# Kernel optimization log

Measured on AMD Instinct MI355X. Metric: run time of the kernel, lower is better.

## Reference

```python
import jax, jax.numpy as jnp
import numpy as np

B, D, H, S, E = 16384, 512, 1024, 8, 4
DH = D // 2  # attention hidden


def setup_inputs() -> dict:
    key = jax.random.key(0)
    ks = jax.random.split(key, 20)
    std = 0.1
    return {
        "x": jax.random.normal(ks[0], (B, D), jnp.float32),
        "scenario_ids": jax.random.randint(ks[1], (B,), 0, S, jnp.int32),
        # shared SEI gate
        "gate_w": jax.random.normal(ks[2], (D, E), jnp.float32) * std,
        "gate_b": jnp.zeros((E,), jnp.float32),
        # shared sub-experts (stacked): D -> H -> D
        "sub_w1": jax.random.normal(ks[3], (E, D, H), jnp.float32) * std,
        "sub_b1": jnp.zeros((E, H), jnp.float32),
        "sub_w2": jax.random.normal(ks[4], (E, H, D), jnp.float32) * std,
        "sub_b2": jnp.zeros((E, D), jnp.float32),
        # scenario-specific experts (stacked): D -> H -> D
        "spec_w1": jax.random.normal(ks[5], (S, D, H), jnp.float32) * std,
        "spec_b1": jnp.zeros((S, H), jnp.float32),
        "spec_w2": jax.random.normal(ks[6], (S, H, D), jnp.float32) * std,
        "spec_b2": jnp.zeros((S, D), jnp.float32),
        # SAN scenario embeddings + attention MLP (2D -> D/2 -> 1)
        "scen_embed": jax.random.normal(ks[7], (S, D), jnp.float32) * std,
        "attn_w1": jax.random.normal(ks[8], (2 * D, DH), jnp.float32) * std,
        "attn_b1": jnp.zeros((DH,), jnp.float32),
        "attn_w2": jax.random.normal(ks[9], (DH, 1), jnp.float32) * std,
        "attn_b2": jnp.zeros((1,), jnp.float32),
        # SAN output projection (4D -> D)
        "out_w": jax.random.normal(ks[10], (4 * D, D), jnp.float32) * std,
        "out_b": jnp.zeros((D,), jnp.float32),
    }


def reference(x, scenario_ids, gate_w, gate_b, sub_w1, sub_b1, sub_w2, sub_b2,
              spec_w1, spec_b1, spec_w2, spec_b2, scen_embed,
              attn_w1, attn_b1, attn_w2, attn_b2, out_w, out_b):
    b = x.shape[0]
    # --- shared expert (SEI): softmax-gated mixture of E sub-experts ---
    gates = jax.nn.softmax(x @ gate_w + gate_b, axis=-1)            # [B,E]
    h = jax.nn.relu(jnp.einsum('bd,edh->ebh', x, sub_w1) + sub_b1[:, None, :])
    exp_out = jnp.einsum('ebh,ehd->ebd', h, sub_w2) + sub_b2[:, None, :]
    shared = jnp.einsum('be,ebd->bd', gates, exp_out)               # [B,D]
    # --- scenario-specific experts: run all, gather per-sample ---
    hs = jax.nn.relu(jnp.einsum('bd,sdh->sbh', x, spec_w1) + spec_b1[:, None, :])
    spec_all = jnp.einsum('sbh,shd->sbd', hs, spec_w2) + spec_b2[:, None, :]  # [S,B,D]
    specific = spec_all[scenario_ids, jnp.arange(b)]                # [B,D]
    # --- scenario-aware attention (SAN) ---
    # logits[s,b] = MLP(cat([shared[b], scen_embed[s]]))
    s = scen_embed.shape[0]
    comb = jnp.concatenate([
        jnp.broadcast_to(shared[None], (s, b, shared.shape[-1])),
        jnp.broadcast_to(scen_embed[:, None, :], (s, b, scen_embed.shape[-1])),
    ], axis=-1)                                                      # [S,B,2D]
    ah = jax.nn.relu(comb @ attn_w1 + attn_b1)                       # [S,B,D/2]
    logits = (ah @ attn_w2 + attn_b2)[..., 0]                        # [S,B]
    attn_w = jax.nn.softmax(logits.T, axis=-1)                       # [B,S]
    # in the original, all non-current scenario reprs are zeros, so the
    # weighted sums reduce to w[b, sid[b]] * (shared/specific)
    wsel = jnp.take_along_axis(attn_w, scenario_ids[:, None], axis=1)  # [B,1]
    enhanced = jnp.concatenate([shared, wsel * shared, specific, wsel * specific], axis=-1)
    return enhanced @ out_w + out_b                                  # [B,D]
```

## Files before the change

kernel.cpp:

```cpp
#include <hip/hip_runtime.h>
#include <hip/hip_bf16.h>
#include <stdint.h>

typedef __hip_bfloat16 bf16;
typedef __attribute__((ext_vector_type(8))) short short8;
typedef __attribute__((ext_vector_type(4))) short short4v;
typedef __attribute__((ext_vector_type(4))) float f32x4;

constexpr int cB = 16384, cD = 512, cH = 1024, cS = 8, cE = 4, cDH = 256;

__device__ __forceinline__ float tof(bf16 v) { return __bfloat162float(v); }
__device__ __forceinline__ bf16 tob(float v) { return __float2bfloat16(v); }
__device__ __forceinline__ float b2f(short s) {
  uint32_t u = ((uint32_t)(uint16_t)s) << 16;
  return __builtin_bit_cast(float, u);
}
__device__ __forceinline__ float ldf(const void* p, long i, int isbf) {
  return isbf ? b2f(((const short*)p)[i]) : ((const float*)p)[i];
}

__device__ __forceinline__ void gload_lds16(const bf16* g, char* l) {
  __builtin_amdgcn_global_load_lds(
      (const __attribute__((address_space(1))) void*)g,
      (__attribute__((address_space(3))) void*)l, 16, 0, 0);
}

__global__ __launch_bounds__(256) void probe_k(const void* x, int* flag) {
  __shared__ int sh[256];
  const unsigned short* u = (const unsigned short*)x;
  int cnt = 0;
  for (int i = threadIdx.x; i < 2048; i += 256) {
    float v = fabsf(b2f((short)u[2 * i]));
    cnt += (v > 1e-5f && v < 1e3f) ? 1 : 0;
  }
  sh[threadIdx.x] = cnt;
  __syncthreads();
  for (int s = 128; s > 0; s >>= 1) {
    if (threadIdx.x < s) sh[threadIdx.x] += sh[threadIdx.x + s];
    __syncthreads();
  }
  if (threadIdx.x == 0) flag[0] = (sh[0] > 1024) ? 1 : 0;
}

__global__ __launch_bounds__(256) void cvtx_k(const void* x, bf16* xb, const int* flag) {
  int g = blockIdx.x * 256 + threadIdx.x;
  if (flag[0]) {
    ((short8*)xb)[g] = ((const short8*)x)[g];
  } else {
    const f32x4* xf = (const f32x4*)x;
    f32x4 v0 = xf[2 * g], v1 = xf[2 * g + 1];
    short8 o;
#pragma unroll
    for (int j = 0; j < 4; j++) {
      o[j] = __builtin_bit_cast(short, tob(v0[j]));
      o[j + 4] = __builtin_bit_cast(short, tob(v1[j]));
    }
    ((short8*)xb)[g] = o;
  }
}

struct CvtDesc {
  const void* src[11];
  int off[12];
};
__global__ __launch_bounds__(256) void cvt_smalls_k(CvtDesc d, const int* flag, float* dst) {
  int i = blockIdx.x * 256 + threadIdx.x;
  if (i >= d.off[11]) return;
  int isb = flag[0];
  int j = 0;
  while (i >= d.off[j + 1]) j++;
  dst[i] = ldf(d.src[j], i - d.off[j], isb);
}

__global__ __launch_bounds__(256) void transpose_k(const void* in, bf16* out, int ldin, int ldout,
                                                   long in_off, long in_bs, long out_bs,
                                                   const int* flag) {
  __shared__ float tile[32][33];
  int isb = flag[0];
  long src0 = in_off + (long)blockIdx.z * in_bs;
  bf16* dst = out + (long)blockIdx.z * out_bs;
  int c0 = blockIdx.x * 32, r0 = blockIdx.y * 32;
  int tx = threadIdx.x & 31, ty = threadIdx.x >> 5;
#pragma unroll
  for (int i = 0; i < 4; i++)
    tile[ty + i * 8][tx] = ldf(in, src0 + (long)(r0 + ty + i * 8) * ldin + c0 + tx, isb);
  __syncthreads();
#pragma unroll
  for (int i = 0; i < 4; i++)
    dst[(long)(c0 + ty + i * 8) * ldout + r0 + tx] = tob(tile[tx][ty + i * 8]);
}

struct GArgs {
  const bf16* A; int lda;
  const bf16* Bt; int ldb; long bt_stride;
  void* C; int ldc;
  int M, N, K;
  const float* bias; int bias_stride;
  const float* gates; int eidx;
  const int* perm; const int* cum;
  const bf16* P1; const float* wsel;
  const int* dflag;
};

template <int EPI, bool GROUPED, bool GATHER_A, bool SCATTER_C>
__global__ __launch_bounds__(256, 4) void gemm_k(GArgs a) {
  __shared__ char smem[32768];
  char* ldsA = smem;
  char* ldsB = smem + 16384;

  int bxs, bys;
  if constexpr (!GROUPED) {
    const int gx = gridDim.x;
    const int nwg = gx * gridDim.y;
    const int d = blockIdx.y * gx + blockIdx.x;
    const int q = nwg >> 3, r = nwg & 7;
    const int xcd = d & 7, di = d >> 3;
    const int logical = (xcd < r ? xcd * (q + 1) : r * (q + 1) + (xcd - r) * q) + di;
    bxs = logical % gx;
    bys = logical / gx;
  } else {
    bxs = blockIdx.x;
    bys = blockIdx.y;
  }

  int g0, cnt;
  if constexpr (GROUPED) {
    int z = blockIdx.z;
    g0 = a.cum[z];
    cnt = a.cum[z + 1] - g0;
  } else {
    g0 = 0;
    cnt = a.M;
  }
  const int ptile = bys * 128;
  if (ptile >= cnt) return;
  const int n0 = bxs * 128;

  const int t = threadIdx.x, w = t >> 6, l = t & 63;
  const int wm = w >> 1, wn = w & 1;

  const bf16* bt = a.Bt + (GROUPED ? (long)blockIdx.z * a.bt_stride : 0);
  const float* bias = a.bias ? (a.bias + (GROUPED ? blockIdx.z * a.bias_stride : 0)) : nullptr;

  const bf16* aSrc[4];
  const bf16* bSrc[4];
  int ldsOff[4];
#pragma unroll
  for (int c = 0; c < 4; c++) {
    int pos = w * 4096 + c * 1024 + l * 16;
    int row = pos >> 7;
    int su = ((((pos >> 4) & 7) ^ (row & 7))) * 8;
    int p = ptile + row;
    if (p > cnt - 1) p = cnt - 1;
    int ar;
    if constexpr (GATHER_A) ar = a.perm[g0 + p];
    else ar = g0 + p;
    aSrc[c] = a.A + (long)ar * a.lda + su;
    bSrc[c] = bt + (long)(n0 + row) * a.ldb + su;
    ldsOff[c] = w * 4096 + c * 1024;
  }

  f32x4 zero = {0.f, 0.f, 0.f, 0.f};
  f32x4 acc[4][4];
#pragma unroll
  for (int i = 0; i < 4; i++)
#pragma unroll
    for (int j = 0; j < 4; j++) acc[i][j] = zero;

  const int nkt = a.K >> 6;
  for (int kt = 0; kt < nkt; ++kt) {
#pragma unroll
    for (int c = 0; c < 4; c++) gload_lds16(aSrc[c] + kt * 64, ldsA + ldsOff[c]);
#pragma unroll
    for (int c = 0; c < 4; c++) gload_lds16(bSrc[c] + kt * 64, ldsB + ldsOff[c]);
    __syncthreads();
#pragma unroll
    for (int kk = 0; kk < 2; kk++) {
      short8 af[4], bv[4];
#pragma unroll
      for (int mi = 0; mi < 4; mi++) {
        int row = wm * 64 + mi * 16 + (l & 15);
        int kg = kk * 4 + (l >> 4);
        int off = row * 128 + ((kg ^ (row & 7)) << 4);
        af[mi] = *(const short8*)(ldsA + off);
      }
#pragma unroll
      for (int ni = 0; ni < 4; ni++) {
        int row = wn * 64 + ni * 16 + (l & 15);
        int kg = kk * 4 + (l >> 4);
        int off = row * 128 + ((kg ^ (row & 7)) << 4);
        bv[ni] = *(const short8*)(ldsB + off);
      }
#pragma unroll
      for (int mi = 0; mi < 4; mi++)
#pragma unroll
        for (int ni = 0; ni < 4; ni++)
          acc[mi][ni] =
              __builtin_amdgcn_mfma_f32_16x16x32_bf16(af[mi], bv[ni], acc[mi][ni], 0, 0, 0);
    }
    __syncthreads();
  }

  const int l15 = l & 15, lg4 = l >> 4;
  int outbf = 1;
  if constexpr (EPI == 5) outbf = a.dflag[0];
#pragma unroll
  for (int mi = 0; mi < 4; mi++) {
#pragma unroll
    for (int j = 0; j < 4; j++) {
      int p = ptile + wm * 64 + mi * 16 + lg4 * 4 + j;
      if (p >= cnt) continue;
      int crow;
      if constexpr (SCATTER_C) crow = a.perm[g0 + p];
      else crow = g0 + p;
#pragma unroll
      for (int ni = 0; ni < 4; ni++) {
        int n = n0 + wn * 64 + ni * 16 + l15;
        float v = acc[mi][ni][j];
        if constexpr (EPI == 1) {
          v += bias[n];
          v = fmaxf(v, 0.f);
          ((bf16*)a.C)[(long)crow * a.ldc + n] = tob(v);
        } else if constexpr (EPI == 2) {
          float g = a.gates[(long)(g0 + p) * 4 + a.eidx];
          v = g * (v + bias[n]);
          float* Cf = (float*)a.C;
          long idx = (long)crow * a.ldc + n;
          if (a.eidx == 0) Cf[idx] = v;
          else Cf[idx] += v;
        } else if constexpr (EPI == 3) {
          ((float*)a.C)[(long)crow * a.ldc + n] = v;
        } else if constexpr (EPI == 4) {
          v += bias[n];
          ((bf16*)a.C)[(long)crow * a.ldc + n] = tob(v);
        } else if constexpr (EPI == 5) {
          float o = tof(a.P1[(long)crow * a.N + n]) + a.wsel[crow] * v + bias[n];
          if (outbf) ((bf16*)a.C)[(long)crow * a.ldc + n] = tob(o);
          else ((float*)a.C)[(long)crow * a.ldc + n] = o;
        } else if constexpr (EPI == 6) {
          float g = a.gates[(long)(g0 + p) * 4 + (n >> 10)];
          v = g * fmaxf(v + bias[n], 0.f);
          ((bf16*)a.C)[(long)crow * a.ldc + n] = tob(v);
        } else if constexpr (EPI == 7) {
          const float* gr = a.gates + (long)(g0 + p) * 4;
          v += gr[0] * bias[n] + gr[1] * bias[512 + n] + gr[2] * bias[1024 + n] +
               gr[3] * bias[1536 + n];
          ((bf16*)a.C)[(long)crow * a.ldc + n] = tob(v);
        } else if constexpr (EPI == 8) {
          ((bf16*)a.C)[(long)crow * a.ldc + n] = tob(v);
        }
      }
    }
  }
}


__global__ __launch_bounds__(256) void gates_k(const bf16* x, const float* gw, const float* gb,
                                               float* gates) {
  int b = blockIdx.x * 4 + (threadIdx.x >> 6);
  int l = threadIdx.x & 63;
  short8 xv = *(const short8*)(x + (long)b * cD + l * 8);
  float a0 = 0, a1 = 0, a2 = 0, a3 = 0;
#pragma unroll
  for (int j = 0; j < 8; j++) {
    float xf = b2f(xv[j]);
    f32x4 wr = *(const f32x4*)(gw + (l * 8 + j) * 4);
    a0 += xf * wr[0];
    a1 += xf * wr[1];
    a2 += xf * wr[2];
    a3 += xf * wr[3];
  }
#pragma unroll
  for (int o = 32; o > 0; o >>= 1) {
    a0 += __shfl_xor(a0, o);
    a1 += __shfl_xor(a1, o);
    a2 += __shfl_xor(a2, o);
    a3 += __shfl_xor(a3, o);
  }
  a0 += gb[0];
  a1 += gb[1];
  a2 += gb[2];
  a3 += gb[3];
  float m = fmaxf(fmaxf(a0, a1), fmaxf(a2, a3));
  float e0 = expf(a0 - m), e1 = expf(a1 - m), e2 = expf(a2 - m), e3 = expf(a3 - m);
  float s = e0 + e1 + e2 + e3;
  if (l == 0) {
    float* gp = gates + (long)b * 4;
    gp[0] = e0 / s;
    gp[1] = e1 / s;
    gp[2] = e2 / s;
    gp[3] = e3 / s;
  }
}

__global__ __launch_bounds__(256) void bhist_k(const int* sid, int* bh) {
  int blk = blockIdx.x, t = threadIdx.x;
  __shared__ int h[cS];
  if (t < cS) h[t] = 0;
  __syncthreads();
  int s = sid[blk * 256 + t];
#pragma unroll
  for (int q = 0; q < cS; q++) {
    unsigned long long m = __ballot(s == q);
    if ((t & 63) == 0) atomicAdd(&h[q], __popcll(m));
  }
  __syncthreads();
  if (t < cS) bh[blk * cS + t] = h[t];
}

__global__ void bbase_k(const int* bh, int* base, int* cum) {
  __shared__ int tot[cS];
  int s = threadIdx.x;
  if (s < cS) {
    int run = 0;
    for (int b = 0; b < 64; b++) {
      base[b * cS + s] = run;
      run += bh[b * cS + s];
    }
    tot[s] = run;
  }
  __syncthreads();
  if (s == 0) {
    int run = 0;
    for (int q = 0; q < cS; q++) {
      cum[q] = run;
      run += tot[q];
    }
    cum[cS] = run;
  }
  __syncthreads();
  if (s < cS) {
    int c = cum[s];
    for (int b = 0; b < 64; b++) base[b * cS + s] += c;
  }
}

__global__ __launch_bounds__(256) void bscat_k(const int* sid, const int* base, int* perm) {
  int blk = blockIdx.x, t = threadIdx.x, w = t >> 6, l = t & 63;
// ... 33 lines not shown
  red[dg][nl] = a;
  __syncthreads();
  if (dg == 0) {
    float t = b1[n];
#pragma unroll
    for (int g = 0; g < 8; g++) t += red[g][nl];
    scp[s * cDH + n] = t;
  }
}

__global__ __launch_bounds__(256) void wsel_k(const float* sp, const float* scp, const float* w2,
                                              const int* sid, float* wsel) {
  int b = blockIdx.x * 4 + (threadIdx.x >> 6);
  int l = threadIdx.x & 63;
  float spv[4], w2v[4];
#pragma unroll
  for (int q = 0; q < 4; q++) {
    spv[q] = sp[(long)b * cDH + q * 64 + l];
    w2v[q] = w2[q * 64 + l];
  }
  float lg[8];
#pragma unroll
  for (int s = 0; s < 8; s++) {
    float acc = 0.f;
#pragma unroll
    for (int q = 0; q < 4; q++) {
      float v = spv[q] + scp[s * cDH + q * 64 + l];
      v = fmaxf(v, 0.f);
      acc += v * w2v[q];
    }
#pragma unroll
    for (int o = 32; o > 0; o >>= 1) acc += __shfl_xor(acc, o);
    lg[s] = acc;
  }
  float m = lg[0];
#pragma unroll
  for (int s = 1; s < 8; s++) m = fmaxf(m, lg[s]);
  float sum = 0.f;
#pragma unroll
  for (int s = 0; s < 8; s++) sum += expf(lg[s] - m);
  if (l == 0) {
    int s0 = sid[b];
    wsel[b] = expf(lg[s0] - m) / sum;
  }
}

__global__ __launch_bounds__(256) void cvt_shared_k(const float* sf, bf16* ss) {
  int i = blockIdx.x * 256 + threadIdx.x;
  int r = i >> 7, c = (i & 127) * 4;
  f32x4 v = *(const f32x4*)(sf + (long)r * cD + c);
  short4v o;
#pragma unroll
  for (int j = 0; j < 4; j++) o[j] = __builtin_bit_cast(short, tob(v[j]));
  *(short4v*)(ss + (long)r * 1024 + c) = o;
}

extern "C" void kernel_launch(void* const* d_in, const int* in_sizes, int n_in, void* d_out,
                              int out_size, void* d_ws, size_t ws_size, hipStream_t stream) {
  const void* x = d_in[0];
  const int* sid = (const int*)d_in[1];

  char* ws = (char*)d_ws;
  size_t off = 0;
  auto alloc = [&](size_t bytes) -> void* {
    void* p = ws + off;
    off += (bytes + 255) & ~(size_t)255;
    return p;
  };
  int* g_flag = (int*)alloc(64);
  float* g_gates = (float*)alloc((size_t)cB * 4 * 4);
  float* g_wsel = (float*)alloc((size_t)cB * 4);
  int* g_perm = (int*)alloc((size_t)cB * 4);
  int* g_bh = (int*)alloc(64 * cS * 4);
  int* g_base = (int*)alloc(64 * cS * 4);
  int* g_cum = (int*)alloc(64);
  float* g_scp = (float*)alloc((size_t)cS * cDH * 4);
  float* g_small = (float*)alloc((size_t)300000 * 4);
  bf16* g_xb = (bf16*)alloc((size_t)cB * cD * 2);
  bf16* w1t = (bf16*)alloc((size_t)cE * cH * cD * 2);
  bf16* w2cat = (bf16*)alloc((size_t)cD * 4096 * 2);
  bf16* s1t = (bf16*)alloc((size_t)cS * cH * cD * 2);
  bf16* s2t = (bf16*)alloc((size_t)cS * cD * cH * 2);
  bf16* a1t = (bf16*)alloc((size_t)cDH * cD * 2);
  bf16* ow1t = (bf16*)alloc((size_t)cD * 1024 * 2);
  bf16* ow2t = (bf16*)alloc((size_t)cD * 1024 * 2);
  bf16* g_ss = (bf16*)alloc((size_t)cB * 1024 * 2);
  size_t fixed_end = off;
  const size_t MB = 1024ull * 1024ull;
  const bool BIG = (ws_size == 0) || (fixed_end + 135 * MB <= ws_size);
  char* g_big = (char*)alloc(BIG ? 135 * MB : 85 * MB);
  (void)in_sizes;
  (void)n_in;
  (void)out_size;

  dim3 blk(256);
  probe_k<<<1, blk, 0, stream>>>(x, g_flag);
  cvtx_k<<<cB * cD / 8 / 256, blk, 0, stream>>>(x, g_xb, g_flag);

  const int O_GW = 0, O_GB = 2048, O_SB1 = 2052, O_SB2 = 6148, O_PB1 = 8196, O_PB2 = 16388,
            O_EMB = 20484, O_AW1 = 24580, O_AB1 = 286724, O_AW2 = 286980, O_OB = 287236,
            O_END = 287748;
  {
    CvtDesc d;
    const void* srcs[11] = {d_in[2],  d_in[3],  d_in[5],  d_in[7],  d_in[9], d_in[11],
                            d_in[12], d_in[13], d_in[14], d_in[15], d_in[18]};
    int offs[12] = {O_GW, O_GB, O_SB1, O_SB2, O_PB1, O_PB2, O_EMB, O_AW1, O_AB1, O_AW2, O_OB,
                    O_END};
    for (int i = 0; i < 11; i++) d.src[i] = srcs[i];
    for (int i = 0; i < 12; i++) d.off[i] = offs[i];
    cvt_smalls_k<<<(O_END + 255) / 256, blk, 0, stream>>>(d, g_flag, g_small);
  }

  transpose_k<<<dim3(cH / 32, cD / 32, cE), blk, 0, stream>>>(d_in[4], w1t, cH, cD, 0,
                                                              (long)cD * cH, (long)cH * cD, g_flag);
  transpose_k<<<dim3(cD / 32, cH / 32, cE), blk, 0, stream>>>(d_in[6], w2cat, cD, 4096, 0,
                                                              (long)cH * cD, 1024, g_flag);
  transpose_k<<<dim3(cH / 32, cD / 32, cS), blk, 0, stream>>>(d_in[8], s1t, cH, cD, 0,
                                                              (long)cD * cH, (long)cH * cD, g_flag);
  transpose_k<<<dim3(cD / 32, cH / 32, cS), blk, 0, stream>>>(d_in[10], s2t, cD, cH, 0,
                                                              (long)cH * cD, (long)cD * cH, g_flag);
  transpose_k<<<dim3(cDH / 32, cD / 32, 1), blk, 0, stream>>>(d_in[13], a1t, cDH, cD, 0, 0, 0,
                                                              g_flag);
  transpose_k<<<dim3(cD / 32, cD / 32, 1), blk, 0, stream>>>(d_in[17], ow1t, cD, 1024, 0, 0, 0,
                                                             g_flag);
  transpose_k<<<dim3(cD / 32, cD / 32, 1), blk, 0, stream>>>(d_in[17], ow1t + 512, cD, 1024,
                                                             (long)1024 * cD, 0, 0, g_flag);
  transpose_k<<<dim3(cD / 32, cD / 32, 1), blk, 0, stream>>>(d_in[17], ow2t, cD, 1024,
                                                             (long)512 * cD, 0, 0, g_flag);
  transpose_k<<<dim3(cD / 32, cD / 32, 1), blk, 0, stream>>>(d_in[17], ow2t + 512, cD, 1024,
                                                             (long)1536 * cD, 0, 0, g_flag);

  gates_k<<<cB / 4, blk, 0, stream>>>(g_xb, g_small + O_GW, g_small + O_GB, g_gates);
  bhist_k<<<cB / 256, blk, 0, stream>>>(sid, g_bh);
  bbase_k<<<1, 64, 0, stream>>>(g_bh, g_base, g_cum);
  bscat_k<<<cB / 256, blk, 0, stream>>>(sid, g_base, g_perm);

  if (BIG) {
    bf16* h4 = (bf16*)g_big;
    float* sp = (float*)g_big;
    bf16* hspec = (bf16*)g_big;
    bf16* P1 = (bf16*)(g_big + 34 * MB);
    {
      GArgs a{};
      a.A = g_xb; a.lda = cD;
      a.Bt = w1t; a.ldb = cD;
      a.C = h4; a.ldc = 4096;
      a.M = cB; a.N = 4096; a.K = cD;
      a.bias = g_small + O_SB1;
      a.gates = g_gates;
      gemm_k<6, false, false, false><<<dim3(32, cB / 128), blk, 0, stream>>>(a);
    }
    {
      GArgs a{};
      a.A = h4; a.lda = 4096;
      a.Bt = w2cat; a.ldb = 4096;
      a.C = g_ss; a.ldc = 1024;
      a.M = cB; a.N = cD; a.K = 4096;
      a.bias = g_small + O_SB2;
      a.gates = g_gates;
      gemm_k<7, false, false, false><<<dim3(cD / 128, cB / 128), blk, 0, stream>>>(a);
    }
    {
      GArgs a{};
      a.A = g_ss; a.lda = 1024;
      a.Bt = a1t; a.ldb = cD;
      a.C = sp; a.ldc = cDH;
      a.M = cB; a.N = cDH; a.K = cD;
      gemm_k<3, false, false, false><<<dim3(cDH / 128, cB / 128), blk, 0, stream>>>(a);
    }
    scenpart_k<<<dim3(cS, 8), blk, 0, stream>>>(g_small + O_EMB, g_small + O_AW1, g_small + O_AB1,
                                                g_scp);
    wsel_k<<<cB / 4, blk, 0, stream>>>(sp, g_scp, g_small + O_AW2, sid, g_wsel);
    {
      GArgs a{};
      a.A = g_xb; a.lda = cD;
      a.Bt = s1t; a.ldb = cD; a.bt_stride = (long)cH * cD;
      a.C = hspec; a.ldc = cH;
      a.M = cB; a.N = cH; a.K = cD;
      a.bias = g_small + O_PB1; a.bias_stride = cH;
      a.perm = g_perm; a.cum = g_cum;
      gemm_k<1, true, true, false><<<dim3(cH / 128, cB / 128, cS), blk, 0, stream>>>(a);
    }
    {
      GArgs a{};
      a.A = hspec; a.lda = cH;
      a.Bt = s2t; a.ldb = cH; a.bt_stride = (long)cD * cH;
      a.C = g_ss + 512; a.ldc = 1024;
      a.M = cB; a.N = cD; a.K = cH;
      a.bias = g_small + O_PB2; a.bias_stride = cD;
      a.perm = g_perm; a.cum = g_cum;
      gemm_k<4, true, false, true><<<dim3(cD / 128, cB / 128, cS), blk, 0, stream>>>(a);
    }
    {
      GArgs a{};
      a.A = g_ss; a.lda = 1024;
      a.Bt = ow1t; a.ldb = 1024;
      a.C = P1; a.ldc = cD;
      a.M = cB; a.N = cD; a.K = 1024;
      gemm_k<8, false, false, false><<<dim3(cD / 128, cB / 128), blk, 0, stream>>>(a);
    }
    {
      GArgs a{};
      a.A = g_ss; a.lda = 1024;
      a.Bt = ow2t; a.ldb = 1024;
      a.C = d_out; a.ldc = cD;
      a.M = cB; a.N = cD; a.K = 1024;
      a.bias = g_small + O_OB;
      a.P1 = P1; a.wsel = g_wsel; a.dflag = g_flag;
      gemm_k<5, false, false, false><<<dim3(cD / 128, cB / 128), blk, 0, stream>>>(a);
    }
  } else {
    float* f32a = (float*)g_big;
    bf16* hbuf = (bf16*)(g_big + 34 * MB);
    bf16* P1b = (bf16*)(g_big + 68 * MB);
    for (int e = 0; e < cE; e++) {
      GArgs a1{};
      a1.A = g_xb; a1.lda = cD;
      a1.Bt = w1t + (size_t)e * cH * cD; a1.ldb = cD;
      a1.C = hbuf; a1.ldc = cH;
      a1.M = cB; a1.N = cH; a1.K = cD;
      a1.bias = g_small + O_SB1 + e * cH;
      gemm_k<1, false, false, false><<<dim3(cH / 128, cB / 128), blk, 0, stream>>>(a1);
      GArgs a2{};
      a2.A = hbuf; a2.lda = cH;
      a2.Bt = w2cat + (size_t)e * 1024; a2.ldb = 4096;
      a2.C = f32a; a2.ldc = cD;
      a2.M = cB; a2.N = cD; a2.K = cH;
      a2.bias = g_small + O_SB2 + e * cD;
      a2.gates = g_gates; a2.eidx = e;
      gemm_k<2, false, false, false><<<dim3(cD / 128, cB / 128), blk, 0, stream>>>(a2);
    }
    cvt_shared_k<<<cB * 128 / 256, blk, 0, stream>>>(f32a, g_ss);
    {
      GArgs a{};
      a.A = g_xb; a.lda = cD;
      a.Bt = s1t; a.ldb = cD; a.bt_stride = (long)cH * cD;
      a.C = hbuf; a.ldc = cH;
      a.M = cB; a.N = cH; a.K = cD;
      a.bias = g_small + O_PB1; a.bias_stride = cH;
      a.perm = g_perm; a.cum = g_cum;
      gemm_k<1, true, true, false><<<dim3(cH / 128, cB / 128, cS), blk, 0, stream>>>(a);
    }
    {
      GArgs a{};
      a.A = hbuf; a.lda = cH;
      a.Bt = s2t; a.ldb = cH; a.bt_stride = (long)cD * cH;
      a.C = g_ss + 512; a.ldc = 1024;
      a.M = cB; a.N = cD; a.K = cH;
      a.bias = g_small + O_PB2; a.bias_stride = cD;
      a.perm = g_perm; a.cum = g_cum;
      gemm_k<4, true, false, true><<<dim3(cD / 128, cB / 128, cS), blk, 0, stream>>>(a);
    }
    {
      GArgs a{};
      a.A = g_ss; a.lda = 1024;
      a.Bt = a1t; a.ldb = cD;
      a.C = f32a; a.ldc = cDH;
      a.M = cB; a.N = cDH; a.K = cD;
      gemm_k<3, false, false, false><<<dim3(cDH / 128, cB / 128), blk, 0, stream>>>(a);
    }
    scenpart_k<<<dim3(cS, 8), blk, 0, stream>>>(g_small + O_EMB, g_small + O_AW1, g_small + O_AB1,
                                                g_scp);
    wsel_k<<<cB / 4, blk, 0, stream>>>(f32a, g_scp, g_small + O_AW2, sid, g_wsel);
    {
      GArgs a{};
      a.A = g_ss; a.lda = 1024;
      a.Bt = ow1t; a.ldb = 1024;
      a.C = P1b; a.ldc = cD;
      a.M = cB; a.N = cD; a.K = 1024;
      gemm_k<8, false, false, false><<<dim3(cD / 128, cB / 128), blk, 0, stream>>>(a);
    }
    {
      GArgs a{};
      a.A = g_ss; a.lda = 1024;
      a.Bt = ow2t; a.ldb = 1024;
      a.C = d_out; a.ldc = cD;
      a.M = cB; a.N = cD; a.K = 1024;
      a.bias = g_small + O_OB;
      a.P1 = P1b; a.wsel = g_wsel; a.dflag = g_flag;
      gemm_k<5, false, false, false><<<dim3(cD / 128, cB / 128), blk, 0, stream>>>(a);
    }
  }
}
```

Baseline: 460.9 us.

## Add 256x256-tile 512-thread GEMM kernel for dense stages with XCD remap

Adds a new GEMM kernel using 256x256 output tiles, 8 waves, double-buffered direct-to-LDS loads with XOR swizzle, priority-boosted MFMA blocks and an XCD-aware workgroup remapping. It replaces the 128x128 GEMMs for the shared-expert up/down projections and the two output-projection GEMMs on the big-workspace path. Larger tiles raise arithmetic intensity and cut redundant global traffic. The cost is 128KB LDS, one block per CU, and fewer blocks (128 for N=512 GEMMs), which may underfill the GPU.

```diff
diff --git a/kernel.cpp b/kernel.cpp
--- a/kernel.cpp
+++ b/kernel.cpp
@@ -254,6 +254,177 @@
   }
 }
 
+struct G6Args {
+  const bf16* A;
+  const bf16* Bt;
+  void* C;
+  int N, K, ldc;
+  const float* bias;
+  const float* gates;
+  const bf16* P1;
+  const float* wsel;
+  const int* dflag;
+};
+
+template <int EPI>
+__global__ __launch_bounds__(512, 1) void gemm256_k(G6Args a) {
+  extern __shared__ char sm[];
+  const int t = threadIdx.x, w = t >> 6, l = t & 63;
+  const int wm = w >> 2, wn = w & 3;
+
+  const int gx = gridDim.x;
+  const int nwg = gx * gridDim.y;
+  const int d = blockIdx.y * gx + blockIdx.x;
+  const int q = nwg >> 3, r = nwg & 7;
+  const int xcd = d & 7, di = d >> 3;
+  const int logical = (xcd < r ? xcd * (q + 1) : r * (q + 1) + (xcd - r) * q) + di;
+  const int m0 = (logical / gx) * 256, n0 = (logical % gx) * 256;
+
+  const bf16* aS[4];
+  const bf16* bS[4];
+  int ldsO[4];
+#pragma unroll
+  for (int c = 0; c < 4; c++) {
+    int pos = c * 8192 + t * 16;
+    int row = pos >> 7;
+    int su = (((pos >> 4) & 7) ^ (row & 7)) * 8;
+    aS[c] = a.A + (long)(m0 + row) * a.K + su;
+    bS[c] = a.Bt + (long)(n0 + row) * a.K + su;
+    ldsO[c] = c * 8192 + (w << 10);
+  }
+  auto stage = [&](int kt, int bb) {
+#pragma unroll
+    for (int c = 0; c < 4; c++) gload_lds16(aS[c] + kt * 64, sm + bb * 65536 + ldsO[c]);
+#pragma unroll
+    for (int c = 0; c < 4; c++) gload_lds16(bS[c] + kt * 64, sm + bb * 65536 + 32768 + ldsO[c]);
+  };
+  auto rdA = [&](int bb, int mi, int kk) -> short8 {
+    int row = wm * 128 + mi * 16 + (l & 15);
+    int kg = kk * 4 + (l >> 4);
+    return *(const short8*)(sm + bb * 65536 + row * 128 + ((kg ^ (row & 7)) << 4));
+  };
+  auto rdB = [&](int bb, int ni, int kk) -> short8 {
+    int row = wn * 64 + ni * 16 + (l & 15);
+    int kg = kk * 4 + (l >> 4);
+    return *(const short8*)(sm + bb * 65536 + 32768 + row * 128 + ((kg ^ (row & 7)) << 4));
+  };
+
+  f32x4 acc[8][4];
+#pragma unroll
+  for (int i = 0; i < 8; i++)
+#pragma unroll
+    for (int j = 0; j < 4; j++) acc[i][j] = {0.f, 0.f, 0.f, 0.f};
+
+  const int nkt = a.K >> 6;
+  stage(0, 0);
+  stage(1, 1);
+
+  for (int kt = 0; kt < nkt; ++kt) {
+    const int bb = kt & 1;
+    if (kt + 1 < nkt) {
+      asm volatile("s_waitcnt vmcnt(8)" ::: "memory");
+    } else {
+      asm volatile("s_waitcnt vmcnt(0)" ::: "memory");
+    }
+    __builtin_amdgcn_sched_barrier(0);
+    __builtin_amdgcn_s_barrier();
+    __builtin_amdgcn_sched_barrier(0);
+
+    short8 fa[4][2], fb0[2][2], fb1[2][2];
+#pragma unroll
+    for (int mi = 0; mi < 4; mi++)
+#pragma unroll
+      for (int kk = 0; kk < 2; kk++) fa[mi][kk] = rdA(bb, mi, kk);
+#pragma unroll
+    for (int ni = 0; ni < 2; ni++)
+#pragma unroll
+      for (int kk = 0; kk < 2; kk++) fb0[ni][kk] = rdB(bb, ni, kk);
+    __builtin_amdgcn_s_setprio(1);
+#pragma unroll
+    for (int mi = 0; mi < 4; mi++)
+#pragma unroll
+      for (int ni = 0; ni < 2; ni++)
+#pragma unroll
+        for (int kk = 0; kk < 2; kk++)
+          acc[mi][ni] = __builtin_amdgcn_mfma_f32_16x16x32_bf16(fa[mi][kk], fb0[ni][kk],
+                                                                acc[mi][ni], 0, 0, 0);
+    __builtin_amdgcn_s_setprio(0);
+#pragma unroll
+    for (int ni = 0; ni < 2; ni++)
+#pragma unroll
+      for (int kk = 0; kk < 2; kk++) fb1[ni][kk] = rdB(bb, ni + 2, kk);
+    __builtin_amdgcn_s_setprio(1);
+#pragma unroll
+    for (int mi = 0; mi < 4; mi++)
+#pragma unroll
+      for (int ni = 0; ni < 2; ni++)
+#pragma unroll
+        for (int kk = 0; kk < 2; kk++)
+          acc[mi][ni + 2] = __builtin_amdgcn_mfma_f32_16x16x32_bf16(fa[mi][kk], fb1[ni][kk],
+                                                                    acc[mi][ni + 2], 0, 0, 0);
+    __builtin_amdgcn_s_setprio(0);
+#pragma unroll
+    for (int mi = 0; mi < 4; mi++)
+#pragma unroll
+      for (int kk = 0; kk < 2; kk++) fa[mi][kk] = rdA(bb, mi + 4, kk);
+    __builtin_amdgcn_s_setprio(1);
+#pragma unroll
+    for (int mi = 0; mi < 4; mi++)
+#pragma unroll
+      for (int ni = 0; ni < 2; ni++)
+#pragma unroll
+        for (int kk = 0; kk < 2; kk++)
+          acc[mi + 4][ni] = __builtin_amdgcn_mfma_f32_16x16x32_bf16(fa[mi][kk], fb0[ni][kk],
+                                                                    acc[mi + 4][ni], 0, 0, 0);
+    __builtin_amdgcn_s_setprio(0);
+    __builtin_amdgcn_s_setprio(1);
+#pragma unroll
+    for (int mi = 0; mi < 4; mi++)
+#pragma unroll
+      for (int ni = 0; ni < 2; ni++)
+#pragma unroll
+        for (int kk = 0; kk < 2; kk++)
+          acc[mi + 4][ni + 2] = __builtin_amdgcn_mfma_f32_16x16x32_bf16(fa[mi][kk], fb1[ni][kk],
+                                                                        acc[mi + 4][ni + 2], 0, 0, 0);
+    __builtin_amdgcn_s_setprio(0);
+
+    __builtin_amdgcn_s_barrier();
+    __builtin_amdgcn_sched_barrier(0);
+    if (kt + 2 < nkt) stage(kt + 2, bb);
+  }
+
+  const int l15 = l & 15, lg4 = l >> 4;
+  int outbf = 1;
+  if constexpr (EPI == 5) outbf = a.dflag[0];
+#pragma unroll
+  for (int mi = 0; mi < 8; mi++) {
+#pragma unroll
+    for (int j = 0; j < 4; j++) {
+      int crow = m0 + wm * 128 + mi * 16 + lg4 * 4 + j;
+#pragma unroll
+      for (int ni = 0; ni < 4; ni++) {
+        int n = n0 + wn * 64 + ni * 16 + l15;
+        float v = acc[mi][ni][j];
+        if constexpr (EPI == 6) {
+          float g = a.gates[(long)crow * 4 + (n >> 10)];
+          v = g * fmaxf(v + a.bias[n], 0.f);
+          ((bf16*)a.C)[(long)crow * a.ldc + n] = tob(v);
+        } else if constexpr (EPI == 7) {
+          const float* gr = a.gates + (long)crow * 4;
+          v += gr[0] * a.bias[n] + gr[1] * a.bias[512 + n] + gr[2] * a.bias[1024 + n] +
+               gr[3] * a.bias[1536 + n];
+          ((bf16*)a.C)[(long)crow * a.ldc + n] = tob(v);
+        } else if constexpr (EPI == 8) {
+          ((bf16*)a.C)[(long)crow * a.ldc + n] = tob(v);
+        } else if constexpr (EPI == 5) {
+          float o = tof(a.P1[(long)crow * a.N + n]) + a.wsel[crow] * v + a.bias[n];
+          if (outbf) ((bf16*)a.C)[(long)crow * a.ldc + n] = tob(o);
+          else ((float*)a.C)[(long)crow * a.ldc + n] = o;
+        }
+      }
+    }
+  }
+}
 
 __global__ __launch_bounds__(256) void gates_k(const bf16* x, const float* gw, const float* gb,
                                                float* gates) {
@@ -464,6 +635,16 @@
   (void)n_in;
   (void)out_size;
 
+  bool use256 = true;
+  use256 &= hipFuncSetAttribute(reinterpret_cast<const void*>(gemm256_k<6>),
+                                hipFuncAttributeMaxDynamicSharedMemorySize, 131072) == hipSuccess;
+  use256 &= hipFuncSetAttribute(reinterpret_cast<const void*>(gemm256_k<7>),
+                                hipFuncAttributeMaxDynamicSharedMemorySize, 131072) == hipSuccess;
+  use256 &= hipFuncSetAttribute(reinterpret_cast<const void*>(gemm256_k<8>),
+                                hipFuncAttributeMaxDynamicSharedMemorySize, 131072) == hipSuccess;
+  use256 &= hipFuncSetAttribute(reinterpret_cast<const void*>(gemm256_k<5>),
+                                hipFuncAttributeMaxDynamicSharedMemorySize, 131072) == hipSuccess;
+
   dim3 blk(256);
   probe_k<<<1, blk, 0, stream>>>(x, g_flag);
   cvtx_k<<<cB * cD / 8 / 256, blk, 0, stream>>>(x, g_xb, g_flag);
@@ -511,32 +692,37 @@
     float* sp = (float*)g_big;
     bf16* hspec = (bf16*)g_big;
     bf16* P1 = (bf16*)(g_big + 34 * MB);
+
+    if (use256) {
+      G6Args a{};
+      a.A = g_xb; a.Bt = w1t; a.C = h4;
+      a.N = 4096; a.K = cD; a.ldc = 4096;
+      a.bias = g_small + O_SB1; a.gates = g_gates;
+      gemm256_k<6><<<dim3(16, 64), 512, 131072, stream>>>(a);
+    } else {
+      GArgs a{};
+      a.A = g_xb; a.lda = cD; a.Bt = w1t; a.ldb = cD;
+      a.C = h4; a.ldc = 4096; a.M = cB; a.N = 4096; a.K = cD;
+      a.bias = g_small + O_SB1; a.gates = g_gates;
+      gemm_k<6, false, false, false><<<dim3(32, cB / 128), blk, 0, stream>>>(a);
+    }
+    if (use256) {
+      G6Args a{};
+      a.A = h4; a.Bt = w2cat; a.C = g_ss;
+      a.N = cD; a.K = 4096; a.ldc = 1024;
+      a.bias = g_small + O_SB2; a.gates = g_gates;
+      gemm256_k<7><<<dim3(2, 64), 512, 131072, stream>>>(a);
+    } else {
+      GArgs a{};
+      a.A = h4; a.lda = 4096; a.Bt = w2cat; a.ldb = 4096;
+      a.C = g_ss; a.ldc = 1024; a.M = cB; a.N = cD; a.K = 4096;
+      a.bias = g_small + O_SB2; a.gates = g_gates;
+      gemm_k<7, false, false, false><<<dim3(cD / 128, cB / 128), blk, 0, stream>>>(a);
+    }
     {
       GArgs a{};
-      a.A = g_xb; a.lda = cD;
-      a.Bt = w1t; a.ldb = cD;
-      a.C = h4; a.ldc = 4096;
-      a.M = cB; a.N = 4096; a.K = cD;
-      a.bias = g_small + O_SB1;
-      a.gates = g_gates;
-      gemm_k<6, false, false, false><<<dim3(32, cB / 128), blk, 0, stream>>>(a);
-    }
-    {
-      GArgs a{};
-      a.A = h4; a.lda = 4096;
-      a.Bt = w2cat; a.ldb = 4096;
-      a.C = g_ss; a.ldc = 1024;
-      a.M = cB; a.N = cD; a.K = 4096;
-      a.bias = g_small + O_SB2;
-      a.gates = g_gates;
-      gemm_k<7, false, false, false><<<dim3(cD / 128, cB / 128), blk, 0, stream>>>(a);
-    }
-    {
-      GArgs a{};
-      a.A = g_ss; a.lda = 1024;
-      a.Bt = a1t; a.ldb = cD;
-      a.C = sp; a.ldc = cDH;
-      a.M = cB; a.N = cDH; a.K = cD;
+      a.A = g_ss; a.lda = 1024; a.Bt = a1t; a.ldb = cD;
+      a.C = sp; a.ldc = cDH; a.M = cB; a.N = cDH; a.K = cD;
       gemm_k<3, false, false, false><<<dim3(cDH / 128, cB / 128), blk, 0, stream>>>(a);
     }
     scenpart_k<<<dim3(cS, 8), blk, 0, stream>>>(g_small + O_EMB, g_small + O_AW1, g_small + O_AB1,
@@ -544,40 +730,42 @@
     wsel_k<<<cB / 4, blk, 0, stream>>>(sp, g_scp, g_small + O_AW2, sid, g_wsel);
     {
       GArgs a{};
-      a.A = g_xb; a.lda = cD;
-      a.Bt = s1t; a.ldb = cD; a.bt_stride = (long)cH * cD;
-      a.C = hspec; a.ldc = cH;
-      a.M = cB; a.N = cH; a.K = cD;
+      a.A = g_xb; a.lda = cD; a.Bt = s1t; a.ldb = cD; a.bt_stride = (long)cH * cD;
+      a.C = hspec; a.ldc = cH; a.M = cB; a.N = cH; a.K = cD;
       a.bias = g_small + O_PB1; a.bias_stride = cH;
       a.perm = g_perm; a.cum = g_cum;
       gemm_k<1, true, true, false><<<dim3(cH / 128, cB / 128, cS), blk, 0, stream>>>(a);
     }
     {
       GArgs a{};
-      a.A = hspec; a.lda = cH;
-      a.Bt = s2t; a.ldb = cH; a.bt_stride = (long)cD * cH;
-      a.C = g_ss + 512; a.ldc = 1024;
-      a.M = cB; a.N = cD; a.K = cH;
+      a.A = hspec; a.lda = cH; a.Bt = s2t; a.ldb = cH; a.bt_stride = (long)cD * cH;
+      a.C = g_ss + 512; a.ldc = 1024; a.M = cB; a.N = cD; a.K = cH;
       a.bias = g_small + O_PB2; a.bias_stride = cD;
       a.perm = g_perm; a.cum = g_cum;
       gemm_k<4, true, false, true><<<dim3(cD / 128, cB / 128, cS), blk, 0, stream>>>(a);
     }
-    {
-      GArgs a{};
-      a.A = g_ss; a.lda = 1024;
-      a.Bt = ow1t; a.ldb = 1024;
-      a.C = P1; a.ldc = cD;
-      a.M = cB; a.N = cD; a.K = 1024;
+    if (use256) {
+      G6Args a{};
+      a.A = g_ss; a.Bt = ow1t; a.C = P1;
+      a.N = cD; a.K = 1024; a.ldc = cD;
+      gemm256_k<8><<<dim3(2, 64), 512, 131072, stream>>>(a);
+    } else {
+      GArgs a{};
+      a.A = g_ss; a.lda = 1024; a.Bt = ow1t; a.ldb = 1024;
+      a.C = P1; a.ldc = cD; a.M = cB; a.N = cD; a.K = 1024;
       gemm_k<8, false, false, false><<<dim3(cD / 128, cB / 128), blk, 0, stream>>>(a);
     }
-    {
-      GArgs a{};
-      a.A = g_ss; a.lda = 1024;
-      a.Bt = ow2t; a.ldb = 1024;
-      a.C = d_out; a.ldc = cD;
-      a.M = cB; a.N = cD; a.K = 1024;
-      a.bias = g_small + O_OB;
-      a.P1 = P1; a.wsel = g_wsel; a.dflag = g_flag;
+    if (use256) {
+      G6Args a{};
+      a.A = g_ss; a.Bt = ow2t; a.C = d_out;
+      a.N = cD; a.K = 1024; a.ldc = cD;
+      a.bias = g_small + O_OB; a.P1 = P1; a.wsel = g_wsel; a.dflag = g_flag;
+      gemm256_k<5><<<dim3(2, 64), 512, 131072, stream>>>(a);
+    } else {
+      GArgs a{};
+      a.A = g_ss; a.lda = 1024; a.Bt = ow2t; a.ldb = 1024;
+      a.C = d_out; a.ldc = cD; a.M = cB; a.N = cD; a.K = 1024;
+      a.bias = g_small + O_OB; a.P1 = P1; a.wsel = g_wsel; a.dflag = g_flag;
       gemm_k<5, false, false, false><<<dim3(cD / 128, cB / 128), blk, 0, stream>>>(a);
     }
   } else {
@@ -586,48 +774,37 @@
     bf16* P1b = (bf16*)(g_big + 68 * MB);
     for (int e = 0; e < cE; e++) {
       GArgs a1{};
-      a1.A = g_xb; a1.lda = cD;
-      a1.Bt = w1t + (size_t)e * cH * cD; a1.ldb = cD;
-      a1.C = hbuf; a1.ldc = cH;
-      a1.M = cB; a1.N = cH; a1.K = cD;
+      a1.A = g_xb; a1.lda = cD; a1.Bt = w1t + (size_t)e * cH * cD; a1.ldb = cD;
+      a1.C = hbuf; a1.ldc = cH; a1.M = cB; a1.N = cH; a1.K = cD;
       a1.bias = g_small + O_SB1 + e * cH;
       gemm_k<1, false, false, false><<<dim3(cH / 128, cB / 128), blk, 0, stream>>>(a1);
       GArgs a2{};
-      a2.A = hbuf; a2.lda = cH;
-      a2.Bt = w2cat + (size_t)e * 1024; a2.ldb = 4096;
-      a2.C = f32a; a2.ldc = cD;
-      a2.M = cB; a2.N = cD; a2.K = cH;
-      a2.bias = g_small + O_SB2 + e * cD;
-      a2.gates = g_gates; a2.eidx = e;
+      a2.A = hbuf; a2.lda = cH; a2.Bt = w2cat + (size_t)e * 1024; a2.ldb = 4096;
+      a2.C = f32a; a2.ldc = cD; a2.M = cB; a2.N = cD; a2.K = cH;
+      a2.bias = g_small + O_SB2 + e * cD; a2.gates = g_gates; a2.eidx = e;
       gemm_k<2, false, false, false><<<dim3(cD / 128, cB / 128), blk, 0, stream>>>(a2);
     }
     cvt_shared_k<<<cB * 128 / 256, blk, 0, stream>>>(f32a, g_ss);
     {
       GArgs a{};
-      a.A = g_xb; a.lda = cD;
-      a.Bt = s1t; a.ldb = cD; a.bt_stride = (long)cH * cD;
-      a.C = hbuf; a.ldc = cH;
-      a.M = cB; a.N = cH; a.K = cD;
+      a.A = g_xb; a.lda = cD; a.Bt = s1t; a.ldb = cD; a.bt_stride = (long)cH * cD;
+      a.C = hbuf; a.ldc = cH; a.M = cB; a.N = cH; a.K = cD;
       a.bias = g_small + O_PB1; a.bias_stride = cH;
       a.perm = g_perm; a.cum = g_cum;
       gemm_k<1, true, true, false><<<dim3(cH / 128, cB / 128, cS), blk, 0, stream>>>(a);
     }
     {
       GArgs a{};
-      a.A = hbuf; a.lda = cH;
-      a.Bt = s2t; a.ldb = cH; a.bt_stride = (long)cD * cH;
-      a.C = g_ss + 512; a.ldc = 1024;
-      a.M = cB; a.N = cD; a.K = cH;
+      a.A = hbuf; a.lda = cH; a.Bt = s2t; a.ldb = cH; a.bt_stride = (long)cD * cH;
+      a.C = g_ss + 512; a.ldc = 1024; a.M = cB; a.N = cD; a.K = cH;
       a.bias = g_small + O_PB2; a.bias_stride = cD;
       a.perm = g_perm; a.cum = g_cum;
       gemm_k<4, true, false, true><<<dim3(cD / 128, cB / 128, cS), blk, 0, stream>>>(a);
     }
     {
       GArgs a{};
-      a.A = g_ss; a.lda = 1024;
-      a.Bt = a1t; a.ldb = cD;
-      a.C = f32a; a.ldc = cDH;
-      a.M = cB; a.N = cDH; a.K = cD;
+      a.A = g_ss; a.lda = 1024; a.Bt = a1t; a.ldb = cD;
+      a.C = f32a; a.ldc = cDH; a.M = cB; a.N = cDH; a.K = cD;
       gemm_k<3, false, false, false><<<dim3(cDH / 128, cB / 128), blk, 0, stream>>>(a);
     }
     scenpart_k<<<dim3(cS, 8), blk, 0, stream>>>(g_small + O_EMB, g_small + O_AW1, g_small + O_AB1,
@@ -635,20 +812,15 @@
     wsel_k<<<cB / 4, blk, 0, stream>>>(f32a, g_scp, g_small + O_AW2, sid, g_wsel);
     {
       GArgs a{};
-      a.A = g_ss; a.lda = 1024;
-      a.Bt = ow1t; a.ldb = 1024;
-      a.C = P1b; a.ldc = cD;
-      a.M = cB; a.N = cD; a.K = 1024;
+      a.A = g_ss; a.lda = 1024; a.Bt = ow1t; a.ldb = 1024;
+      a.C = P1b; a.ldc = cD; a.M = cB; a.N = cD; a.K = 1024;
       gemm_k<8, false, false, false><<<dim3(cD / 128, cB / 128), blk, 0, stream>>>(a);
     }
     {
       GArgs a{};
-      a.A = g_ss; a.lda = 1024;
-      a.Bt = ow2t; a.ldb = 1024;
-      a.C = d_out; a.ldc = cD;
-      a.M = cB; a.N = cD; a.K = 1024;
-      a.bias = g_small + O_OB;
-      a.P1 = P1b; a.wsel = g_wsel; a.dflag = g_flag;
+      a.A = g_ss; a.lda = 1024; a.Bt = ow2t; a.ldb = 1024;
+      a.C = d_out; a.ldc = cD; a.M = cB; a.N = cD; a.K = 1024;
+      a.bias = g_small + O_OB; a.P1 = P1b; a.wsel = g_wsel; a.dflag = g_flag;
       gemm_k<5, false, false, false><<<dim3(cD / 128, cB / 128), blk, 0, stream>>>(a);
     }
   }
```

Result: slower. 573.6 us (+24.5%).

## Fuse the two output-projection GEMMs using an interleaved paired weight layout

Applied to the files above, without the earlier changes.

The two output-projection GEMMs (unscaled part P1 and wsel-scaled part) become one GEMM with N=1024 over a new interleaved weight layout. Each wave's accumulator tiles then hold both halves for the same output column, so the epilogue combines them as acc0 + wsel*acc1 + bias. This removes the bf16 P1 intermediate write and read-back plus one kernel launch, and the four weight transposes are merged into a single kernel. The hidden-activation epilogues also switch to nontemporal stores, which may help or hurt depending on whether those values are re-read from cache soon after.

```diff
diff --git a/kernel.cpp b/kernel.cpp
--- a/kernel.cpp
+++ b/kernel.cpp
@@ -17,6 +17,9 @@
 }
 __device__ __forceinline__ float ldf(const void* p, long i, int isbf) {
   return isbf ? b2f(((const short*)p)[i]) : ((const float*)p)[i];
+}
+__device__ __forceinline__ void stbf_nt(bf16* p, float v) {
+  __builtin_nontemporal_store(__builtin_bit_cast(short, tob(v)), (short*)p);
 }
 
 __device__ __forceinline__ void gload_lds16(const bf16* g, char* l) {
@@ -90,6 +93,26 @@
     dst[(long)(c0 + ty + i * 8) * ldout + r0 + tx] = tob(tile[tx][ty + i * 8]);
 }
 
+__global__ __launch_bounds__(256) void owt_k(const void* ow, bf16* owpair, const int* flag) {
+  __shared__ float tile[32][33];
+  int isb = flag[0];
+  int z = blockIdx.z;
+  int m = z & 1, kb = (z >> 1) * 512;
+  long base = (long)z * 512 * cD;
+  int c0 = blockIdx.x * 32, r0 = blockIdx.y * 32;
+  int tx = threadIdx.x & 31, ty = threadIdx.x >> 5;
+#pragma unroll
+  for (int i = 0; i < 4; i++)
+    tile[ty + i * 8][tx] = ldf(ow, base + (long)(r0 + ty + i * 8) * cD + c0 + tx, isb);
+  __syncthreads();
+#pragma unroll
+  for (int i = 0; i < 4; i++) {
+    int n = c0 + ty + i * 8;
+    int R = ((n >> 6) << 7) + (((n >> 5) & 1) << 6) + (m << 5) + (((n >> 4) & 1) << 4) + (n & 15);
+    owpair[(long)R * 1024 + kb + r0 + tx] = tob(tile[tx][ty + i * 8]);
+  }
+}
+
 struct GArgs {
   const bf16* A; int lda;
   const bf16* Bt; int ldb; long bt_stride;
@@ -98,7 +121,7 @@
   const float* bias; int bias_stride;
   const float* gates; int eidx;
   const int* perm; const int* cum;
-  const bf16* P1; const float* wsel;
+  const float* wsel;
   const int* dflag;
 };
 
@@ -203,7 +226,7 @@
 
   const int l15 = l & 15, lg4 = l >> 4;
   int outbf = 1;
-  if constexpr (EPI == 5) outbf = a.dflag[0];
+  if constexpr (EPI == 9) outbf = a.dflag[0];
 #pragma unroll
   for (int mi = 0; mi < 4; mi++) {
 #pragma unroll
@@ -213,6 +236,17 @@
       int crow;
       if constexpr (SCATTER_C) crow = a.perm[g0 + p];
       else crow = g0 + p;
+      if constexpr (EPI == 9) {
+        float wv = a.wsel[crow];
+#pragma unroll
+        for (int ni = 0; ni < 2; ni++) {
+          int n = (n0 >> 1) + wn * 32 + ni * 16 + l15;
+          float o = acc[mi][ni][j] + wv * acc[mi][ni + 2][j] + a.bias[n];
+          if (outbf) ((bf16*)a.C)[(long)crow * a.ldc + n] = tob(o);
+          else ((float*)a.C)[(long)crow * a.ldc + n] = o;
+        }
+        continue;
+      }
 #pragma unroll
       for (int ni = 0; ni < 4; ni++) {
         int n = n0 + wn * 64 + ni * 16 + l15;
@@ -220,7 +254,7 @@
         if constexpr (EPI == 1) {
           v += bias[n];
           v = fmaxf(v, 0.f);
-          ((bf16*)a.C)[(long)crow * a.ldc + n] = tob(v);
+          stbf_nt(&((bf16*)a.C)[(long)crow * a.ldc + n], v);
         } else if constexpr (EPI == 2) {
           float g = a.gates[(long)(g0 + p) * 4 + a.eidx];
           v = g * (v + bias[n]);
@@ -233,27 +267,20 @@
         } else if constexpr (EPI == 4) {
           v += bias[n];
           ((bf16*)a.C)[(long)crow * a.ldc + n] = tob(v);
-        } else if constexpr (EPI == 5) {
-          float o = tof(a.P1[(long)crow * a.N + n]) + a.wsel[crow] * v + bias[n];
-          if (outbf) ((bf16*)a.C)[(long)crow * a.ldc + n] = tob(o);
-          else ((float*)a.C)[(long)crow * a.ldc + n] = o;
         } else if constexpr (EPI == 6) {
           float g = a.gates[(long)(g0 + p) * 4 + (n >> 10)];
           v = g * fmaxf(v + bias[n], 0.f);
-          ((bf16*)a.C)[(long)crow * a.ldc + n] = tob(v);
+          stbf_nt(&((bf16*)a.C)[(long)crow * a.ldc + n], v);
         } else if constexpr (EPI == 7) {
           const float* gr = a.gates + (long)(g0 + p) * 4;
           v += gr[0] * bias[n] + gr[1] * bias[512 + n] + gr[2] * bias[1024 + n] +
                gr[3] * bias[1536 + n];
           ((bf16*)a.C)[(long)crow * a.ldc + n] = tob(v);
-        } else if constexpr (EPI == 8) {
-          ((bf16*)a.C)[(long)crow * a.ldc + n] = tob(v);
         }
       }
     }
   }
 }
-
 
 __global__ __launch_bounds__(256) void gates_k(const bf16* x, const float* gw, const float* gb,
                                                float* gates) {
@@ -453,13 +480,12 @@
   bf16* s1t = (bf16*)alloc((size_t)cS * cH * cD * 2);
   bf16* s2t = (bf16*)alloc((size_t)cS * cD * cH * 2);
   bf16* a1t = (bf16*)alloc((size_t)cDH * cD * 2);
-  bf16* ow1t = (bf16*)alloc((size_t)cD * 1024 * 2);
-  bf16* ow2t = (bf16*)alloc((size_t)cD * 1024 * 2);
+  bf16* owpair = (bf16*)alloc((size_t)1024 * 1024 * 2);
   bf16* g_ss = (bf16*)alloc((size_t)cB * 1024 * 2);
   size_t fixed_end = off;
   const size_t MB = 1024ull * 1024ull;
   const bool BIG = (ws_size == 0) || (fixed_end + 135 * MB <= ws_size);
-  char* g_big = (char*)alloc(BIG ? 135 * MB : 85 * MB);
+  char* g_big = (char*)alloc(BIG ? 135 * MB : 68 * MB);
   (void)in_sizes;
   (void)n_in;
   (void)out_size;
@@ -492,14 +518,7 @@
                                                               (long)cH * cD, (long)cD * cH, g_flag);
   transpose_k<<<dim3(cDH / 32, cD / 32, 1), blk, 0, stream>>>(d_in[13], a1t, cDH, cD, 0, 0, 0,
                                                               g_flag);
-  transpose_k<<<dim3(cD / 32, cD / 32, 1), blk, 0, stream>>>(d_in[17], ow1t, cD, 1024, 0, 0, 0,
-                                                             g_flag);
-  transpose_k<<<dim3(cD / 32, cD / 32, 1), blk, 0, stream>>>(d_in[17], ow1t + 512, cD, 1024,
-                                                             (long)1024 * cD, 0, 0, g_flag);
-  transpose_k<<<dim3(cD / 32, cD / 32, 1), blk, 0, stream>>>(d_in[17], ow2t, cD, 1024,
-                                                             (long)512 * cD, 0, 0, g_flag);
-  transpose_k<<<dim3(cD / 32, cD / 32, 1), blk, 0, stream>>>(d_in[17], ow2t + 512, cD, 1024,
-                                                             (long)1536 * cD, 0, 0, g_flag);
+  owt_k<<<dim3(cD / 32, cD / 32, 4), blk, 0, stream>>>(d_in[17], owpair, g_flag);
 
   gates_k<<<cB / 4, blk, 0, stream>>>(g_xb, g_small + O_GW, g_small + O_GB, g_gates);
   bhist_k<<<cB / 256, blk, 0, stream>>>(sid, g_bh);
@@ -510,33 +529,24 @@
     bf16* h4 = (bf16*)g_big;
     float* sp = (float*)g_big;
     bf16* hspec = (bf16*)g_big;
-    bf16* P1 = (bf16*)(g_big + 34 * MB);
-    {
-      GArgs a{};
-      a.A = g_xb; a.lda = cD;
-      a.Bt = w1t; a.ldb = cD;
-      a.C = h4; a.ldc = 4096;
-      a.M = cB; a.N = 4096; a.K = cD;
-      a.bias = g_small + O_SB1;
-      a.gates = g_gates;
+    {
+      GArgs a{};
+      a.A = g_xb; a.lda = cD; a.Bt = w1t; a.ldb = cD;
+      a.C = h4; a.ldc = 4096; a.M = cB; a.N = 4096; a.K = cD;
+      a.bias = g_small + O_SB1; a.gates = g_gates;
       gemm_k<6, false, false, false><<<dim3(32, cB / 128), blk, 0, stream>>>(a);
     }
     {
       GArgs a{};
-      a.A = h4; a.lda = 4096;
-      a.Bt = w2cat; a.ldb = 4096;
-      a.C = g_ss; a.ldc = 1024;
-      a.M = cB; a.N = cD; a.K = 4096;
-      a.bias = g_small + O_SB2;
-      a.gates = g_gates;
+      a.A = h4; a.lda = 4096; a.Bt = w2cat; a.ldb = 4096;
+      a.C = g_ss; a.ldc = 1024; a.M = cB; a.N = cD; a.K = 4096;
+      a.bias = g_small + O_SB2; a.gates = g_gates;
       gemm_k<7, false, false, false><<<dim3(cD / 128, cB / 128), blk, 0, stream>>>(a);
     }
     {
       GArgs a{};
-      a.A = g_ss; a.lda = 1024;
-      a.Bt = a1t; a.ldb = cD;
-      a.C = sp; a.ldc = cDH;
-      a.M = cB; a.N = cDH; a.K = cD;
+      a.A = g_ss; a.lda = 1024; a.Bt = a1t; a.ldb = cD;
+      a.C = sp; a.ldc = cDH; a.M = cB; a.N = cDH; a.K = cD;
       gemm_k<3, false, false, false><<<dim3(cDH / 128, cB / 128), blk, 0, stream>>>(a);
     }
     scenpart_k<<<dim3(cS, 8), blk, 0, stream>>>(g_small + O_EMB, g_small + O_AW1, g_small + O_AB1,
@@ -544,90 +554,63 @@
     wsel_k<<<cB / 4, blk, 0, stream>>>(sp, g_scp, g_small + O_AW2, sid, g_wsel);
     {
       GArgs a{};
-      a.A = g_xb; a.lda = cD;
-      a.Bt = s1t; a.ldb = cD; a.bt_stride = (long)cH * cD;
-      a.C = hspec; a.ldc = cH;
-      a.M = cB; a.N = cH; a.K = cD;
+      a.A = g_xb; a.lda = cD; a.Bt = s1t; a.ldb = cD; a.bt_stride = (long)cH * cD;
+      a.C = hspec; a.ldc = cH; a.M = cB; a.N = cH; a.K = cD;
       a.bias = g_small + O_PB1; a.bias_stride = cH;
       a.perm = g_perm; a.cum = g_cum;
       gemm_k<1, true, true, false><<<dim3(cH / 128, cB / 128, cS), blk, 0, stream>>>(a);
     }
     {
       GArgs a{};
-      a.A = hspec; a.lda = cH;
-      a.Bt = s2t; a.ldb = cH; a.bt_stride = (long)cD * cH;
-      a.C = g_ss + 512; a.ldc = 1024;
-      a.M = cB; a.N = cD; a.K = cH;
+      a.A = hspec; a.lda = cH; a.Bt = s2t; a.ldb = cH; a.bt_stride = (long)cD * cH;
+      a.C = g_ss + 512; a.ldc = 1024; a.M = cB; a.N = cD; a.K = cH;
       a.bias = g_small + O_PB2; a.bias_stride = cD;
       a.perm = g_perm; a.cum = g_cum;
       gemm_k<4, true, false, true><<<dim3(cD / 128, cB / 128, cS), blk, 0, stream>>>(a);
     }
     {
       GArgs a{};
-      a.A = g_ss; a.lda = 1024;
-      a.Bt = ow1t; a.ldb = 1024;
-      a.C = P1; a.ldc = cD;
-      a.M = cB; a.N = cD; a.K = 1024;
-      gemm_k<8, false, false, false><<<dim3(cD / 128, cB / 128), blk, 0, stream>>>(a);
-    }
-    {
-      GArgs a{};
-      a.A = g_ss; a.lda = 1024;
-      a.Bt = ow2t; a.ldb = 1024;
-      a.C = d_out; a.ldc = cD;
-      a.M = cB; a.N = cD; a.K = 1024;
-      a.bias = g_small + O_OB;
-      a.P1 = P1; a.wsel = g_wsel; a.dflag = g_flag;
-      gemm_k<5, false, false, false><<<dim3(cD / 128, cB / 128), blk, 0, stream>>>(a);
+      a.A = g_ss; a.lda = 1024; a.Bt = owpair; a.ldb = 1024;
+      a.C = d_out; a.ldc = cD; a.M = cB; a.N = 1024; a.K = 1024;
+      a.bias = g_small + O_OB; a.wsel = g_wsel; a.dflag = g_flag;
+      gemm_k<9, false, false, false><<<dim3(8, cB / 128), blk, 0, stream>>>(a);
     }
   } else {
     float* f32a = (float*)g_big;
     bf16* hbuf = (bf16*)(g_big + 34 * MB);
-    bf16* P1b = (bf16*)(g_big + 68 * MB);
     for (int e = 0; e < cE; e++) {
       GArgs a1{};
-      a1.A = g_xb; a1.lda = cD;
-      a1.Bt = w1t + (size_t)e * cH * cD; a1.ldb = cD;
-      a1.C = hbuf; a1.ldc = cH;
-      a1.M = cB; a1.N = cH; a1.K = cD;
+      a1.A = g_xb; a1.lda = cD; a1.Bt = w1t + (size_t)e * cH * cD; a1.ldb = cD;
+      a1.C = hbuf; a1.ldc = cH; a1.M = cB; a1.N = cH; a1.K = cD;
       a1.bias = g_small + O_SB1 + e * cH;
       gemm_k<1, false, false, false><<<dim3(cH / 128, cB / 128), blk, 0, stream>>>(a1);
       GArgs a2{};
-      a2.A = hbuf; a2.lda = cH;
-      a2.Bt = w2cat + (size_t)e * 1024; a2.ldb = 4096;
-      a2.C = f32a; a2.ldc = cD;
-      a2.M = cB; a2.N = cD; a2.K = cH;
-      a2.bias = g_small + O_SB2 + e * cD;
-      a2.gates = g_gates; a2.eidx = e;
+      a2.A = hbuf; a2.lda = cH; a2.Bt = w2cat + (size_t)e * 1024; a2.ldb = 4096;
+      a2.C = f32a; a2.ldc = cD; a2.M = cB; a2.N = cD; a2.K = cH;
+      a2.bias = g_small + O_SB2 + e * cD; a2.gates = g_gates; a2.eidx = e;
       gemm_k<2, false, false, false><<<dim3(cD / 128, cB / 128), blk, 0, stream>>>(a2);
     }
     cvt_shared_k<<<cB * 128 / 256, blk, 0, stream>>>(f32a, g_ss);
     {
       GArgs a{};
-      a.A = g_xb; a.lda = cD;
-      a.Bt = s1t; a.ldb = cD; a.bt_stride = (long)cH * cD;
-      a.C = hbuf; a.ldc = cH;
-      a.M = cB; a.N = cH; a.K = cD;
+      a.A = g_xb; a.lda = cD; a.Bt = s1t; a.ldb = cD; a.bt_stride = (long)cH * cD;
+      a.C = hbuf; a.ldc = cH; a.M = cB; a.N = cH; a.K = cD;
       a.bias = g_small + O_PB1; a.bias_stride = cH;
       a.perm = g_perm; a.cum = g_cum;
       gemm_k<1, true, true, false><<<dim3(cH / 128, cB / 128, cS), blk, 0, stream>>>(a);
     }
     {
       GArgs a{};
-      a.A = hbuf; a.lda = cH;
-      a.Bt = s2t; a.ldb = cH; a.bt_stride = (long)cD * cH;
-      a.C = g_ss + 512; a.ldc = 1024;
-      a.M = cB; a.N = cD; a.K = cH;
+      a.A = hbuf; a.lda = cH; a.Bt = s2t; a.ldb = cH; a.bt_stride = (long)cD * cH;
+      a.C = g_ss + 512; a.ldc = 1024; a.M = cB; a.N = cD; a.K = cH;
       a.bias = g_small + O_PB2; a.bias_stride = cD;
       a.perm = g_perm; a.cum = g_cum;
       gemm_k<4, true, false, true><<<dim3(cD / 128, cB / 128, cS), blk, 0, stream>>>(a);
     }
     {
       GArgs a{};
-      a.A = g_ss; a.lda = 1024;
-      a.Bt = a1t; a.ldb = cD;
-      a.C = f32a; a.ldc = cDH;
-      a.M = cB; a.N = cDH; a.K = cD;
+      a.A = g_ss; a.lda = 1024; a.Bt = a1t; a.ldb = cD;
+      a.C = f32a; a.ldc = cDH; a.M = cB; a.N = cDH; a.K = cD;
       gemm_k<3, false, false, false><<<dim3(cDH / 128, cB / 128), blk, 0, stream>>>(a);
     }
     scenpart_k<<<dim3(cS, 8), blk, 0, stream>>>(g_small + O_EMB, g_small + O_AW1, g_small + O_AB1,
@@ -635,21 +618,10 @@
     wsel_k<<<cB / 4, blk, 0, stream>>>(f32a, g_scp, g_small + O_AW2, sid, g_wsel);
     {
       GArgs a{};
-      a.A = g_ss; a.lda = 1024;
-      a.Bt = ow1t; a.ldb = 1024;
-      a.C = P1b; a.ldc = cD;
-      a.M = cB; a.N = cD; a.K = 1024;
-      gemm_k<8, false, false, false><<<dim3(cD / 128, cB / 128), blk, 0, stream>>>(a);
-    }
-    {
-      GArgs a{};
-      a.A = g_ss; a.lda = 1024;
-      a.Bt = ow2t; a.ldb = 1024;
-      a.C = d_out; a.ldc = cD;
-      a.M = cB; a.N = cD; a.K = 1024;
-      a.bias = g_small + O_OB;
-      a.P1 = P1b; a.wsel = g_wsel; a.dflag = g_flag;
-      gemm_k<5, false, false, false><<<dim3(cD / 128, cB / 128), blk, 0, stream>>>(a);
-    }
-  }
-}
+      a.A = g_ss; a.lda = 1024; a.Bt = owpair; a.ldb = 1024;
+      a.C = d_out; a.ldc = cD; a.M = cB; a.N = 1024; a.K = 1024;
+      a.bias = g_small + O_OB; a.wsel = g_wsel; a.dflag = g_flag;
+      gemm_k<9, false, false, false><<<dim3(8, cB / 128), blk, 0, stream>>>(a);
+    }
+  }
+}
```

New measurement: 412.5 us. 10.5% less time.
